# Optimization experiments

Measured on AMD Instinct MI355X. Metric: run time of the kernel, lower is better.

Reference implementation:

```python
import jax, jax.numpy as jnp
import numpy as np

B, L, D = 4096, 200, 128


def setup_inputs() -> dict:
    key = jax.random.key(0)
    ks = jax.random.split(key, 9)
    s_in = 1.0 / np.sqrt(2 * D)  # torch Linear default init scale (uniform bound)
    inp = {
        "h_states": jax.random.normal(ks[0], (B, L, D), dtype=jnp.float32),
        "target_emb_proj": jax.random.normal(ks[1], (B, D), dtype=jnp.float32),
        "mask": jax.random.randint(ks[2], (B, L), 0, 2).astype(bool),
        "W_r": jax.random.uniform(ks[3], (2 * D, D), jnp.float32, -s_in, s_in),
        "b_r": jax.random.uniform(ks[4], (D,), jnp.float32, -s_in, s_in),
        "W_u": jax.random.uniform(ks[5], (2 * D, D), jnp.float32, -s_in, s_in),
        "b_u": jax.random.uniform(ks[6], (D,), jnp.float32, -s_in, s_in),
        "W_h": jax.random.uniform(ks[7], (2 * D, D), jnp.float32, -s_in, s_in),
        "b_h": jax.random.uniform(ks[8], (D,), jnp.float32, -s_in, s_in),
    }
    return inp


def reference(h_states, target_emb_proj, mask, W_r, b_r, W_u, b_u, W_h, b_h):
    Bd, Ld, Dd = h_states.shape
    # target-aware attention scores over history: (B, L)
    scores = jnp.einsum("bld,bd->bl", h_states, target_emb_proj) / np.sqrt(Dd).astype(h_states.dtype)
    scores = jnp.where(mask, scores, jnp.asarray(-1e9, scores.dtype))
    attn = jax.nn.softmax(scores, axis=-1)  # (B, L)

    xs = (
        jnp.transpose(h_states, (1, 0, 2)),  # (L, B, D)
        attn.T,                               # (L, B)
        mask.T,                               # (L, B)
    )

    def step(h, x):
        x_t, e_t, m_t = x
        combined = jnp.concatenate([x_t, h], axis=-1)  # (B, 2D)
        r = jax.nn.sigmoid(combined @ W_r + b_r)
        u = jax.nn.sigmoid(combined @ W_u + b_u)
        u_prime = e_t[:, None] * u
        h_tilde = jnp.tanh(jnp.concatenate([x_t, r * h], axis=-1) @ W_h + b_h)
        h_new = (1.0 - u_prime) * h + u_prime * h_tilde
        h_next = jnp.where(m_t[:, None], h_new, h)
        return h_next, None

    h0 = jnp.zeros((Bd, Dd), dtype=h_states.dtype)
    h_final, _ = jax.lax.scan(step, h0, xs)
    return h_final
```

## Files before the change

### kernel.cpp

```cpp
#include <hip/hip_runtime.h>
#include <hip/hip_bf16.h>
#include <stdint.h>

#define LSEQ 200
#define DDIM 128

typedef __attribute__((ext_vector_type(8))) __bf16 bf16x8;
typedef __attribute__((ext_vector_type(4))) float f32x4;

__device__ __forceinline__ float fast_exp(float x) {
  return __builtin_amdgcn_exp2f(x * 1.4426950408889634f);
}
__device__ __forceinline__ float fast_sigmoid(float x) {
  return __builtin_amdgcn_rcpf(1.0f + fast_exp(-x));
}
__device__ __forceinline__ float fast_tanh(float x) {
  float ax = __builtin_fabsf(x);
  float t = __builtin_amdgcn_exp2f(ax * -2.885390081777927f);
  float r = (1.0f - t) * __builtin_amdgcn_rcpf(1.0f + t);
  return x < 0.0f ? -r : r;
}
__device__ __forceinline__ f32x4 mfma16(bf16x8 a, bf16x8 b, f32x4 c) {
  return __builtin_amdgcn_mfma_f32_16x16x32_bf16(a, b, c, 0, 0, 0);
}

__global__ __launch_bounds__(512) void k_scores(
    const float* __restrict__ h_states, const float* __restrict__ target,
    const int* __restrict__ mask, uint4* __restrict__ xp,
    float* __restrict__ attnT, int B) {
  __shared__ float s_sc[4][16][LSEQ];
  __shared__ float s_tgt[16][DDIM];
  const int b16 = blockIdx.x;
  const int bb = b16 * 16;
  const int tid = threadIdx.x;
  for (int i = tid; i < 16 * DDIM; i += 512)
    s_tgt[i >> 7][i & 127] = target[(size_t)(bb + (i >> 7)) * DDIM + (i & 127)];
  __syncthreads();

  {
    const int lane = tid & 63;
    const int kt = (tid >> 6) & 3;
    const int tp = tid >> 8;
    const int row = lane & 15;
    const int hi = lane >> 4;
    const int kbase = kt * 32 + hi * 8;
    const float* src = h_states + ((size_t)(bb + row) * LSEQ) * DDIM + kbase;
    const float* tg = &s_tgt[row][kbase];
#pragma unroll 2
    for (int t = tp; t < LSEQ; t += 2) {
      float4 a = *(const float4*)(src + (size_t)t * DDIM);
      float4 b = *(const float4*)(src + (size_t)t * DDIM + 4);
      float dv = (a.x * tg[0] + a.y * tg[1] + a.z * tg[2] + a.w * tg[3]) +
                 (b.x * tg[4] + b.y * tg[5] + b.z * tg[6] + b.w * tg[7]);
      dv += __shfl_xor(dv, 16);
      dv += __shfl_xor(dv, 32);
      if (hi == 0) s_sc[kt][row][t] = dv;
      union { __bf16 h[8]; uint4 v; } pk;
      pk.h[0] = (__bf16)a.x; pk.h[1] = (__bf16)a.y; pk.h[2] = (__bf16)a.z; pk.h[3] = (__bf16)a.w;
      pk.h[4] = (__bf16)b.x; pk.h[5] = (__bf16)b.y; pk.h[6] = (__bf16)b.z; pk.h[7] = (__bf16)b.w;
      xp[(((size_t)b16 * LSEQ + t) * 4 + kt) * 64 + lane] = pk.v;
    }
  }
  __syncthreads();

  if (tid < 256) {
    const int r2 = tid >> 4;
    const int j = tid & 15;
    const int* mrow = mask + (size_t)(bb + r2) * LSEQ;
    float mx = -3.0e38f;
    for (int t = j; t < LSEQ; t += 16) {
      float s = (s_sc[0][r2][t] + s_sc[1][r2][t]) + (s_sc[2][r2][t] + s_sc[3][r2][t]);
      s *= 0.088388347648318447f;
      s = (mrow[t] != 0) ? s : -3.0e38f;
      s_sc[0][r2][t] = s;
      mx = fmaxf(mx, s);
    }
    mx = fmaxf(mx, __shfl_xor(mx, 1));
    mx = fmaxf(mx, __shfl_xor(mx, 2));
    mx = fmaxf(mx, __shfl_xor(mx, 4));
    mx = fmaxf(mx, __shfl_xor(mx, 8));
    float se = 0.0f;
    for (int t = j; t < LSEQ; t += 16) {
      float e = fast_exp(s_sc[0][r2][t] - mx);
      s_sc[1][r2][t] = e;
      se += e;
    }
    se += __shfl_xor(se, 1);
    se += __shfl_xor(se, 2);
    se += __shfl_xor(se, 4);
    se += __shfl_xor(se, 8);
    float rs = __builtin_amdgcn_rcpf(se);
    for (int t = j; t < LSEQ; t += 16)
      attnT[((size_t)b16 * LSEQ + t) * 16 + r2] =
          (mrow[t] != 0) ? s_sc[1][r2][t] * rs : 0.0f;
  }
}

#define STEP(t, XC, XN, AXRC, AXUC, AXHC, AXRN, AXUN, AXHN)                  \
  do {                                                                       \
    if ((t) + 2 < LSEQ) {                                                    \
      _Pragma("unroll") for (int kt = 0; kt < 4; ++kt)                       \
          XN[kt] = xpb[((size_t)(t) + 2) * 256 + kt * 64];                   \
    }                                                                        \
    float att = s_att[(t)][rA];                                              \
    bf16x8 hf[4];                                                            \
    _Pragma("unroll") for (int kt = 0; kt < 4; ++kt)                         \
        hf[kt] = __builtin_bit_cast(bf16x8, s_hb_f[kt][lane]);               \
    if ((t) + 1 < LSEQ) {         \
      AXRN = vbr;                                                            \
      AXUN = vbu;                                                            \
      _Pragma("unroll") for (int kt = 0; kt < 4; ++kt) {                     \
        bf16x8 b = __builtin_bit_cast(bf16x8, XC[kt]);                       \
        AXRN = mfma16(wr[kt], b, AXRN);                                      \
        AXUN = mfma16(wu[kt], b, AXUN);                                      \
      }                                                                      \
    }                                                                        \
    f32x4 r1 = AXRC, u1 = AXUC;                                              \
    f32x4 r2 = {0.f, 0.f, 0.f, 0.f}, u2 = {0.f, 0.f, 0.f, 0.f};              \
    r1 = mfma16(wr[4], hf[0], r1); u1 = mfma16(wu[4], hf[0], u1);            \
    r2 = mfma16(wr[6], hf[2], r2); u2 = mfma16(wu[6], hf[2], u2);            \
    r1 = mfma16(wr[5], hf[1], r1); u1 = mfma16(wu[5], hf[1], u1);            \
    r2 = mfma16(wr[7], hf[3], r2); u2 = mfma16(wu[7], hf[3], u2);            \
    f32x4 accr = r1 + r2, accu = u1 + u2;                                    \
    float rr[4], uu[4];                                                      \
    union { __bf16 h[4]; uint2 v; } rhv;                                     \
    _Pragma("unroll") for (int j = 0; j < 4; ++j) {                          \
      rr[j] = fast_sigmoid(accr[j]);                                         \
      uu[j] = fast_sigmoid(accu[j]);                                         \
      rhv.h[j] = (__bf16)(rr[j] * hD[j]);                                    \
    }                                                                        \
    *rh_w = rhv.v;                                                           \
    asm volatile("s_waitcnt lgkmcnt(0)" ::: "memory");                       \
    __builtin_amdgcn_s_barrier();                                            \
    __builtin_amdgcn_sched_barrier(0);                                       \
    bf16x8 rf[4];                                                            \
    _Pragma("unroll") for (int kt = 0; kt < 4; ++kt)                         \
        rf[kt] = __builtin_bit_cast(bf16x8, s_rh_f[kt][lane]);               \
    if ((t) + 1 < LSEQ) {                                                    \
      AXHN = vbh;                                                            \
      _Pragma("unroll") for (int kt = 0; kt < 4; ++kt)                       \
          AXHN = mfma16(wh[kt], __builtin_bit_cast(bf16x8, XC[kt]), AXHN);   \
    }                                                                        \
    f32x4 h1 = AXHC, h2 = {0.f, 0.f, 0.f, 0.f};                              \
    h1 = mfma16(wh[4], rf[0], h1);                                           \
    h2 = mfma16(wh[6], rf[2], h2);                                           \
    h1 = mfma16(wh[5], rf[1], h1);                                           \
    h2 = mfma16(wh[7], rf[3], h2);                                           \
    f32x4 acch = h1 + h2;                                                    \
    union { __bf16 h[4]; uint2 v; } hbv;                                     \
    _Pragma("unroll") for (int j = 0; j < 4; ++j) {                          \
      float ht = fast_tanh(acch[j]);                                         \
      float up = att * uu[j];                                                \
      hD[j] += up * (ht - hD[j]);                                            \
      hbv.h[j] = (__bf16)hD[j];                                              \
    }                                                                        \
    *hb_w = hbv.v;                                                           \
    asm volatile("s_waitcnt lgkmcnt(0)" ::: "memory");                       \
    __builtin_amdgcn_s_barrier();                                            \
    __builtin_amdgcn_sched_barrier(0);                                       \
  } while (0)

__global__ __launch_bounds__(512, 2) void k_recur(
    const uint4* __restrict__ xp, const float* __restrict__ attnT,
    const float* __restrict__ Wr, const float* __restrict__ br,
    const float* __restrict__ Wu, const float* __restrict__ bu,
    const float* __restrict__ Wh, const float* __restrict__ bh,
    float* __restrict__ out, int B) {
  __shared__ uint4 s_hb_f[4][64];
  __shared__ uint4 s_rh_f[4][64];
  __shared__ float s_att[LSEQ][16];
  const int tid = threadIdx.x;
  const int lane = tid & 63;
  const int wv = tid >> 6;
  const int b16 = blockIdx.x;
  const int bb = b16 * 16;
  const int q = lane >> 4;
  const int rA = lane & 15;
  const int col = wv * 16 + rA;

  bf16x8 wr[8], wu[8], wh[8];
#pragma unroll
  for (int kt = 0; kt < 8; ++kt) {
    bf16x8 tr, tu, th;
    int krow = kt * 32 + q * 8;
#pragma unroll
    for (int j = 0; j < 8; ++j) {
      tr[j] = (__bf16)Wr[(size_t)(krow + j) * DDIM + col];
      tu[j] = (__bf16)Wu[(size_t)(krow + j) * DDIM + col];
      th[j] = (__bf16)Wh[(size_t)(krow + j) * DDIM + col];
    }
    wr[kt] = tr; wu[kt] = tu; wh[kt] = th;
  }
  const int cbase = wv * 16 + q * 4;
  f32x4 vbr = {br[cbase], br[cbase + 1], br[cbase + 2], br[cbase + 3]};
  f32x4 vbu = {bu[cbase], bu[cbase + 1], bu[cbase + 2], bu[cbase + 3]};
  f32x4 vbh = {bh[cbase], bh[cbase + 1], bh[cbase + 2], bh[cbase + 3]};

  for (int i = tid; i < LSEQ * 16; i += 512)
    s_att[i >> 4][i & 15] = attnT[(size_t)b16 * LSEQ * 16 + i];
  if (tid < 256) s_hb_f[0][tid & 255] = (uint4){0, 0, 0, 0};

  const int lane_w = rA + 16 * ((wv & 1) * 2 + (q >> 1));
  uint2* hb_w = (uint2*)((char*)s_hb_f + (wv >> 1) * 1024 + lane_w * 16 + (q & 1) * 8);
  uint2* rh_w = (uint2*)((char*)s_rh_f + (wv >> 1) * 1024 + lane_w * 16 + (q & 1) * 8);

  const uint4* xpb = xp + (size_t)b16 * LSEQ * 256 + lane;

  uint4 xT[4], xA[4], xB[4];
#pragma unroll
  for (int kt = 0; kt < 4; ++kt) xT[kt] = xpb[kt * 64];
#pragma unroll
  for (int kt = 0; kt < 4; ++kt) xA[kt] = xpb[256 + kt * 64];
  f32x4 axr0 = vbr, axu0 = vbu, axh0 = vbh;
#pragma unroll
  for (int kt = 0; kt < 4; ++kt) {
    bf16x8 b = __builtin_bit_cast(bf16x8, xT[kt]);
    axr0 = mfma16(wr[kt], b, axr0);
    axu0 = mfma16(wu[kt], b, axu0);
    axh0 = mfma16(wh[kt], b, axh0);
  }
  f32x4 axr1, axu1, axh1;
  float hD[4] = {0.f, 0.f, 0.f, 0.f};
  __syncthreads();

  for (int t = 0; t < LSEQ; t += 2) {
    STEP(t, xA, xB, axr0, axu0, axh0, axr1, axu1, axh1);
    STEP(t + 1, xB, xA, axr1, axu1, axh1, axr0, axu0, axh0);
  }

  float4 o = {hD[0], hD[1], hD[2], hD[3]};
  *(float4*)(out + (size_t)(bb + rA) * DDIM + cbase) = o;
}

extern "C" void kernel_launch(void* const* d_in, const int* in_sizes, int n_in,
                              void* d_out, int out_size, void* d_ws, size_t ws_size,
                              hipStream_t stream) {
  const float* h_states = (const float*)d_in[0];
  const float* target   = (const float*)d_in[1];
  const int*   mask     = (const int*)d_in[2];
  const float* Wr = (const float*)d_in[3];
  const float* br = (const float*)d_in[4];
  const float* Wu = (const float*)d_in[5];
  const float* bu = (const float*)d_in[6];
  const float* Wh = (const float*)d_in[7];
  const float* bh = (const float*)d_in[8];

  const int B = in_sizes[0] / (LSEQ * DDIM);
  uint4* xp = (uint4*)d_ws;
  float* attnT = (float*)((char*)d_ws + (size_t)B * LSEQ * DDIM * 2);

  k_scores<<<B / 16, 512, 0, stream>>>(h_states, target, mask, xp, attnT, B);
  k_recur<<<B / 16, 512, 0, stream>>>(xp, attnT, Wr, br, Wu, bu, Wh, bh,
                                      (float*)d_out, B);
}
```

Baseline: 341.5 us.

## Deepen x prefetch to four steps and interleave input MFMAs around barriers

Grows the register prefetch ring for the input sequence from two to four timesteps so global loads have more steps to land. The input-projection MFMAs for the next step are split so half run before the r*h LDS write and half before the barrier, and the u sigmoid moves after the barrier. Boundary conditionals are dropped in favour of clamped redundant loads and unconditional MFMAs. The scheduler barriers are replaced with a plain compiler memory fence, which lets the compiler move work across the sync point. The cost is higher register pressure at 2 waves per SIMD and some wasted work on the final steps.

```diff
diff --git a/kernel.cpp b/kernel.cpp
--- a/kernel.cpp
+++ b/kernel.cpp
@@ -96,25 +96,29 @@
   }
 }
 
+#define LGKM_BARRIER()                                 \
+  asm volatile("s_waitcnt lgkmcnt(0)" ::: "memory");   \
+  __builtin_amdgcn_s_barrier();                        \
+  asm volatile("" ::: "memory")
+
 #define STEP(t, XC, XN, AXRC, AXUC, AXHC, AXRN, AXUN, AXHN)                  \
   do {                                                                       \
-    if ((t) + 2 < LSEQ) {                                                    \
-      _Pragma("unroll") for (int kt = 0; kt < 4; ++kt)                       \
-          XN[kt] = xpb[((size_t)(t) + 2) * 256 + kt * 64];                   \
-    }                                                                        \
+                                                      \
+    const int tl = ((t) + 4 < LSEQ) ? (t) + 4 : LSEQ - 4;                    \
+    _Pragma("unroll") for (int kt = 0; kt < 4; ++kt)                         \
+        XN[kt] = xpb[(size_t)tl * 256 + kt * 64];                            \
     float att = s_att[(t)][rA];                                              \
     bf16x8 hf[4];                                                            \
     _Pragma("unroll") for (int kt = 0; kt < 4; ++kt)                         \
         hf[kt] = __builtin_bit_cast(bf16x8, s_hb_f[kt][lane]);               \
-    if ((t) + 1 < LSEQ) {         \
-      AXRN = vbr;                                                            \
-      AXUN = vbu;                                                            \
-      _Pragma("unroll") for (int kt = 0; kt < 4; ++kt) {                     \
-        bf16x8 b = __builtin_bit_cast(bf16x8, XC[kt]);                       \
-        AXRN = mfma16(wr[kt], b, AXRN);                                      \
-        AXUN = mfma16(wu[kt], b, AXUN);                                      \
-      }                                                                      \
+                      \
+    AXRN = vbr; AXUN = vbu;                                                  \
+    _Pragma("unroll") for (int kt = 0; kt < 2; ++kt) {                       \
+      bf16x8 b = __builtin_bit_cast(bf16x8, XC[kt]);                         \
+      AXRN = mfma16(wr[kt], b, AXRN);                                        \
+      AXUN = mfma16(wu[kt], b, AXUN);                                        \
     }                                                                        \
+                               \
     f32x4 r1 = AXRC, u1 = AXUC;                                              \
     f32x4 r2 = {0.f, 0.f, 0.f, 0.f}, u2 = {0.f, 0.f, 0.f, 0.f};              \
     r1 = mfma16(wr[4], hf[0], r1); u1 = mfma16(wu[4], hf[0], u1);            \
@@ -122,25 +126,29 @@
     r1 = mfma16(wr[5], hf[1], r1); u1 = mfma16(wu[5], hf[1], u1);            \
     r2 = mfma16(wr[7], hf[3], r2); u2 = mfma16(wu[7], hf[3], u2);            \
     f32x4 accr = r1 + r2, accu = u1 + u2;                                    \
-    float rr[4], uu[4];                                                      \
     union { __bf16 h[4]; uint2 v; } rhv;                                     \
-    _Pragma("unroll") for (int j = 0; j < 4; ++j) {                          \
-      rr[j] = fast_sigmoid(accr[j]);                                         \
+    _Pragma("unroll") for (int j = 0; j < 4; ++j)                            \
+      rhv.h[j] = (__bf16)(fast_sigmoid(accr[j]) * hD[j]);                    \
+    *rh_w = rhv.v;                                                           \
+               \
+    _Pragma("unroll") for (int kt = 2; kt < 4; ++kt) {                       \
+      bf16x8 b = __builtin_bit_cast(bf16x8, XC[kt]);                         \
+      AXRN = mfma16(wr[kt], b, AXRN);                                        \
+      AXUN = mfma16(wu[kt], b, AXUN);                                        \
+    }                                                                        \
+    LGKM_BARRIER();                                                          \
+                                                      \
+    bf16x8 rf[4];                                                            \
+    _Pragma("unroll") for (int kt = 0; kt < 4; ++kt)                         \
+        rf[kt] = __builtin_bit_cast(bf16x8, s_rh_f[kt][lane]);               \
+                        \
+    float uu[4];                                                             \
+    _Pragma("unroll") for (int j = 0; j < 4; ++j)                            \
       uu[j] = fast_sigmoid(accu[j]);                                         \
-      rhv.h[j] = (__bf16)(rr[j] * hD[j]);                                    \
-    }                                                                        \
-    *rh_w = rhv.v;                                                           \
-    asm volatile("s_waitcnt lgkmcnt(0)" ::: "memory");                       \
-    __builtin_amdgcn_s_barrier();                                            \
-    __builtin_amdgcn_sched_barrier(0);                                       \
-    bf16x8 rf[4];                                                            \
-    _Pragma("unroll") for (int kt = 0; kt < 4; ++kt)                         \
-        rf[kt] = __builtin_bit_cast(bf16x8, s_rh_f[kt][lane]);               \
-    if ((t) + 1 < LSEQ) {                                                    \
-      AXHN = vbh;                                                            \
-      _Pragma("unroll") for (int kt = 0; kt < 4; ++kt)                       \
-          AXHN = mfma16(wh[kt], __builtin_bit_cast(bf16x8, XC[kt]), AXHN);   \
-    }                                                                        \
+    AXHN = vbh;                                                              \
+    _Pragma("unroll") for (int kt = 0; kt < 4; ++kt)                         \
+        AXHN = mfma16(wh[kt], __builtin_bit_cast(bf16x8, XC[kt]), AXHN);     \
+                                              \
     f32x4 h1 = AXHC, h2 = {0.f, 0.f, 0.f, 0.f};                              \
     h1 = mfma16(wh[4], rf[0], h1);                                           \
     h2 = mfma16(wh[6], rf[2], h2);                                           \
@@ -155,9 +163,7 @@
       hbv.h[j] = (__bf16)hD[j];                                              \
     }                                                                        \
     *hb_w = hbv.v;                                                           \
-    asm volatile("s_waitcnt lgkmcnt(0)" ::: "memory");                       \
-    __builtin_amdgcn_s_barrier();                                            \
-    __builtin_amdgcn_sched_barrier(0);                                       \
+    LGKM_BARRIER();                                                          \
   } while (0)
 
 __global__ __launch_bounds__(512, 2) void k_recur(
@@ -206,15 +212,20 @@
 
   const uint4* xpb = xp + (size_t)b16 * LSEQ * 256 + lane;
 
-  uint4 xT[4], xA[4], xB[4];
-#pragma unroll
-  for (int kt = 0; kt < 4; ++kt) xT[kt] = xpb[kt * 64];
-#pragma unroll
-  for (int kt = 0; kt < 4; ++kt) xA[kt] = xpb[256 + kt * 64];
+  uint4 xb0[4], xb1[4], xb2[4], xb3[4];
+#pragma unroll
+  for (int kt = 0; kt < 4; ++kt) xb0[kt] = xpb[kt * 64];
+#pragma unroll
+  for (int kt = 0; kt < 4; ++kt) xb1[kt] = xpb[256 + kt * 64];
+#pragma unroll
+  for (int kt = 0; kt < 4; ++kt) xb2[kt] = xpb[512 + kt * 64];
+#pragma unroll
+  for (int kt = 0; kt < 4; ++kt) xb3[kt] = xpb[768 + kt * 64];
+
   f32x4 axr0 = vbr, axu0 = vbu, axh0 = vbh;
 #pragma unroll
   for (int kt = 0; kt < 4; ++kt) {
-    bf16x8 b = __builtin_bit_cast(bf16x8, xT[kt]);
+    bf16x8 b = __builtin_bit_cast(bf16x8, xb0[kt]);
     axr0 = mfma16(wr[kt], b, axr0);
     axu0 = mfma16(wu[kt], b, axu0);
     axh0 = mfma16(wh[kt], b, axh0);
@@ -223,9 +234,11 @@
   float hD[4] = {0.f, 0.f, 0.f, 0.f};
   __syncthreads();
 
-  for (int t = 0; t < LSEQ; t += 2) {
-    STEP(t, xA, xB, axr0, axu0, axh0, axr1, axu1, axh1);
-    STEP(t + 1, xB, xA, axr1, axu1, axh1, axr0, axu0, axh0);
+  for (int t = 0; t < LSEQ; t += 4) {
+    STEP(t + 0, xb1, xb0, axr0, axu0, axh0, axr1, axu1, axh1);
+    STEP(t + 1, xb2, xb1, axr1, axu1, axh1, axr0, axu0, axh0);
+    STEP(t + 2, xb3, xb2, axr0, axu0, axh0, axr1, axu1, axh1);
+    STEP(t + 3, xb0, xb3, axr1, axu1, axh1, axr0, axu0, axh0);
   }
 
   float4 o = {hD[0], hD[1], hD[2], hD[3]};
```

After: 318.2 us. -6.8%, faster.

## Process two independent 16-row batch groups per block to interleave recurrences

Applied to the files above, without the earlier changes.

Each recurrence block now handles 32 batch rows as two independent 16-row chains, issuing their MFMAs interleaved so one chain's work can hide the other's latency within each barrier-separated step. This halves the grid size and the number of barriers per batch row. The input-projection MFMAs are no longer precomputed one step ahead; instead the x loads are prefetched two steps ahead in place. The cost is higher register pressure, fewer blocks (128 instead of 256 on a large GPU), and possible occupancy loss under the 512x2 launch bounds.

```diff
diff --git a/kernel.cpp b/kernel.cpp
--- a/kernel.cpp
+++ b/kernel.cpp
@@ -96,68 +96,85 @@
   }
 }
 
-#define STEP(t, XC, XN, AXRC, AXUC, AXHC, AXRN, AXUN, AXHN)                  \
+#define LGKM_BARRIER()                                 \
+  asm volatile("s_waitcnt lgkmcnt(0)" ::: "memory");   \
+  __builtin_amdgcn_s_barrier();                        \
+  asm volatile("" ::: "memory")
+
+#define STEP(t, XC0, XC1)                                                    \
   do {                                                                       \
-    if ((t) + 2 < LSEQ) {                                                    \
-      _Pragma("unroll") for (int kt = 0; kt < 4; ++kt)                       \
-          XN[kt] = xpb[((size_t)(t) + 2) * 256 + kt * 64];                   \
-    }                                                                        \
-    float att = s_att[(t)][rA];                                              \
-    bf16x8 hf[4];                                                            \
-    _Pragma("unroll") for (int kt = 0; kt < 4; ++kt)                         \
-        hf[kt] = __builtin_bit_cast(bf16x8, s_hb_f[kt][lane]);               \
-    if ((t) + 1 < LSEQ) {         \
-      AXRN = vbr;                                                            \
-      AXUN = vbu;                                                            \
+    float att0 = s_att[(t)][rA];                                             \
+    float att1 = s_att[(t)][16 + rA];                                        \
+    bf16x8 hf0[4], hf1[4];                                                   \
+    _Pragma("unroll") for (int kt = 0; kt < 4; ++kt) {                       \
+      hf0[kt] = __builtin_bit_cast(bf16x8, s_hb_f[0][kt][lane]);             \
+      hf1[kt] = __builtin_bit_cast(bf16x8, s_hb_f[1][kt][lane]);             \
+    }                                                                        \
+    f32x4 r0a = vbr, u0a = vbu, r1a = vbr, u1a = vbu;                        \
+    _Pragma("unroll") for (int kt = 0; kt < 4; ++kt) {   \
+      bf16x8 b0 = __builtin_bit_cast(bf16x8, XC0[kt]);                       \
+      bf16x8 b1 = __builtin_bit_cast(bf16x8, XC1[kt]);                       \
+      r0a = mfma16(wr[kt], b0, r0a);                                         \
+      u0a = mfma16(wu[kt], b0, u0a);                                         \
+      r1a = mfma16(wr[kt], b1, r1a);                                         \
+      u1a = mfma16(wu[kt], b1, u1a);                                         \
+    }                                                                        \
+    f32x4 r0b = {0.f,0.f,0.f,0.f}, u0b = {0.f,0.f,0.f,0.f};                  \
+    f32x4 r1b = {0.f,0.f,0.f,0.f}, u1b = {0.f,0.f,0.f,0.f};                  \
+    _Pragma("unroll") for (int kt = 0; kt < 4; ++kt) {           \
+      r0b = mfma16(wr[4 + kt], hf0[kt], r0b);                                \
+      u0b = mfma16(wu[4 + kt], hf0[kt], u0b);                                \
+      r1b = mfma16(wr[4 + kt], hf1[kt], r1b);                                \
+      u1b = mfma16(wu[4 + kt], hf1[kt], u1b);                                \
+    }                                                                        \
+    f32x4 accr0 = r0a + r0b, accu0 = u0a + u0b;                              \
+    f32x4 accr1 = r1a + r1b, accu1 = u1a + u1b;                              \
+    float uu0[4], uu1[4];                                                    \
+    union { __bf16 h[4]; uint2 v; } rhv0, rhv1;                              \
+    _Pragma("unroll") for (int j = 0; j < 4; ++j) {                          \
+      rhv0.h[j] = (__bf16)(fast_sigmoid(accr0[j]) * hD0[j]);                 \
+      rhv1.h[j] = (__bf16)(fast_sigmoid(accr1[j]) * hD1[j]);                 \
+      uu0[j] = fast_sigmoid(accu0[j]);                                       \
+      uu1[j] = fast_sigmoid(accu1[j]);                                       \
+    }                                                                        \
+    *rh_w0 = rhv0.v;                                                         \
+    *rh_w1 = rhv1.v;                                                         \
+    LGKM_BARRIER();                                                          \
+    bf16x8 rf0[4], rf1[4];                                                   \
+    _Pragma("unroll") for (int kt = 0; kt < 4; ++kt) {                       \
+      rf0[kt] = __builtin_bit_cast(bf16x8, s_rh_f[0][kt][lane]);             \
+      rf1[kt] = __builtin_bit_cast(bf16x8, s_rh_f[1][kt][lane]);             \
+    }                                                                        \
+    f32x4 h0a = vbh, h1a = vbh;                                              \
+    _Pragma("unroll") for (int kt = 0; kt < 4; ++kt) {   \
+      h0a = mfma16(wh[kt], __builtin_bit_cast(bf16x8, XC0[kt]), h0a);        \
+      h1a = mfma16(wh[kt], __builtin_bit_cast(bf16x8, XC1[kt]), h1a);        \
+    }                                                                        \
+    {         \
+      const int tl = ((t) + 2 < LSEQ) ? (t) + 2 : LSEQ - 1;                  \
       _Pragma("unroll") for (int kt = 0; kt < 4; ++kt) {                     \
-        bf16x8 b = __builtin_bit_cast(bf16x8, XC[kt]);                       \
-        AXRN = mfma16(wr[kt], b, AXRN);                                      \
-        AXUN = mfma16(wu[kt], b, AXUN);                                      \
+        XC0[kt] = xpb0[(size_t)tl * 256 + kt * 64];                          \
+        XC1[kt] = xpb1[(size_t)tl * 256 + kt * 64];                          \
       }                                                                      \
     }                                                                        \
-    f32x4 r1 = AXRC, u1 = AXUC;                                              \
-    f32x4 r2 = {0.f, 0.f, 0.f, 0.f}, u2 = {0.f, 0.f, 0.f, 0.f};              \
-    r1 = mfma16(wr[4], hf[0], r1); u1 = mfma16(wu[4], hf[0], u1);            \
-    r2 = mfma16(wr[6], hf[2], r2); u2 = mfma16(wu[6], hf[2], u2);            \
-    r1 = mfma16(wr[5], hf[1], r1); u1 = mfma16(wu[5], hf[1], u1);            \
-    r2 = mfma16(wr[7], hf[3], r2); u2 = mfma16(wu[7], hf[3], u2);            \
-    f32x4 accr = r1 + r2, accu = u1 + u2;                                    \
-    float rr[4], uu[4];                                                      \
-    union { __bf16 h[4]; uint2 v; } rhv;                                     \
+    f32x4 h0b = {0.f,0.f,0.f,0.f}, h1b = {0.f,0.f,0.f,0.f};                  \
+    _Pragma("unroll") for (int kt = 0; kt < 4; ++kt) {           \
+      h0b = mfma16(wh[4 + kt], rf0[kt], h0b);                                \
+      h1b = mfma16(wh[4 + kt], rf1[kt], h1b);                                \
+    }                                                                        \
+    f32x4 acch0 = h0a + h0b, acch1 = h1a + h1b;                              \
+    union { __bf16 h[4]; uint2 v; } hbv0, hbv1;                              \
     _Pragma("unroll") for (int j = 0; j < 4; ++j) {                          \
-      rr[j] = fast_sigmoid(accr[j]);                                         \
-      uu[j] = fast_sigmoid(accu[j]);                                         \
-      rhv.h[j] = (__bf16)(rr[j] * hD[j]);                                    \
-    }                                                                        \
-    *rh_w = rhv.v;                                                           \
-    asm volatile("s_waitcnt lgkmcnt(0)" ::: "memory");                       \
-    __builtin_amdgcn_s_barrier();                                            \
-    __builtin_amdgcn_sched_barrier(0);                                       \
-    bf16x8 rf[4];                                                            \
-    _Pragma("unroll") for (int kt = 0; kt < 4; ++kt)                         \
-        rf[kt] = __builtin_bit_cast(bf16x8, s_rh_f[kt][lane]);               \
-    if ((t) + 1 < LSEQ) {                                                    \
-      AXHN = vbh;                                                            \
-      _Pragma("unroll") for (int kt = 0; kt < 4; ++kt)                       \
-          AXHN = mfma16(wh[kt], __builtin_bit_cast(bf16x8, XC[kt]), AXHN);   \
-    }                                                                        \
-    f32x4 h1 = AXHC, h2 = {0.f, 0.f, 0.f, 0.f};                              \
-    h1 = mfma16(wh[4], rf[0], h1);                                           \
-    h2 = mfma16(wh[6], rf[2], h2);                                           \
-    h1 = mfma16(wh[5], rf[1], h1);                                           \
-    h2 = mfma16(wh[7], rf[3], h2);                                           \
-    f32x4 acch = h1 + h2;                                                    \
-    union { __bf16 h[4]; uint2 v; } hbv;                                     \
-    _Pragma("unroll") for (int j = 0; j < 4; ++j) {                          \
-      float ht = fast_tanh(acch[j]);                                         \
-      float up = att * uu[j];                                                \
-      hD[j] += up * (ht - hD[j]);                                            \
-      hbv.h[j] = (__bf16)hD[j];                                              \
-    }                                                                        \
-    *hb_w = hbv.v;                                                           \
-    asm volatile("s_waitcnt lgkmcnt(0)" ::: "memory");                       \
-    __builtin_amdgcn_s_barrier();                                            \
-    __builtin_amdgcn_sched_barrier(0);                                       \
+      float up0 = att0 * uu0[j];                                             \
+      hD0[j] += up0 * (fast_tanh(acch0[j]) - hD0[j]);                        \
+      hbv0.h[j] = (__bf16)hD0[j];                                            \
+      float up1 = att1 * uu1[j];                                             \
+      hD1[j] += up1 * (fast_tanh(acch1[j]) - hD1[j]);                        \
+      hbv1.h[j] = (__bf16)hD1[j];                                            \
+    }                                                                        \
+    *hb_w0 = hbv0.v;                                                         \
+    *hb_w1 = hbv1.v;                                                         \
+    LGKM_BARRIER();                                                          \
   } while (0)
 
 __global__ __launch_bounds__(512, 2) void k_recur(
@@ -166,14 +183,14 @@
     const float* __restrict__ Wu, const float* __restrict__ bu,
     const float* __restrict__ Wh, const float* __restrict__ bh,
     float* __restrict__ out, int B) {
-  __shared__ uint4 s_hb_f[4][64];
-  __shared__ uint4 s_rh_f[4][64];
-  __shared__ float s_att[LSEQ][16];
+  __shared__ uint4 s_hb_f[2][4][64];
+  __shared__ uint4 s_rh_f[2][4][64];
+  __shared__ float s_att[LSEQ][32];
   const int tid = threadIdx.x;
   const int lane = tid & 63;
   const int wv = tid >> 6;
-  const int b16 = blockIdx.x;
-  const int bb = b16 * 16;
+  const int b32 = blockIdx.x;
+  const int bb = b32 * 32;
   const int q = lane >> 4;
   const int rA = lane & 15;
   const int col = wv * 16 + rA;
@@ -196,40 +213,43 @@
   f32x4 vbu = {bu[cbase], bu[cbase + 1], bu[cbase + 2], bu[cbase + 3]};
   f32x4 vbh = {bh[cbase], bh[cbase + 1], bh[cbase + 2], bh[cbase + 3]};
 
-  for (int i = tid; i < LSEQ * 16; i += 512)
-    s_att[i >> 4][i & 15] = attnT[(size_t)b16 * LSEQ * 16 + i];
-  if (tid < 256) s_hb_f[0][tid & 255] = (uint4){0, 0, 0, 0};
-
-  const int lane_w = rA + 16 * ((wv & 1) * 2 + (q >> 1));
-  uint2* hb_w = (uint2*)((char*)s_hb_f + (wv >> 1) * 1024 + lane_w * 16 + (q & 1) * 8);
-  uint2* rh_w = (uint2*)((char*)s_rh_f + (wv >> 1) * 1024 + lane_w * 16 + (q & 1) * 8);
-
-  const uint4* xpb = xp + (size_t)b16 * LSEQ * 256 + lane;
-
-  uint4 xT[4], xA[4], xB[4];
-#pragma unroll
-  for (int kt = 0; kt < 4; ++kt) xT[kt] = xpb[kt * 64];
-#pragma unroll
-  for (int kt = 0; kt < 4; ++kt) xA[kt] = xpb[256 + kt * 64];
-  f32x4 axr0 = vbr, axu0 = vbu, axh0 = vbh;
+  for (int i = tid; i < LSEQ * 32; i += 512) {
+    int t = i >> 5, gr = (i >> 4) & 1, r = i & 15;
+    s_att[t][gr * 16 + r] =
+        attnT[((size_t)(b32 * 2 + gr) * LSEQ + t) * 16 + r];
+  }
+  ((uint4*)s_hb_f)[tid] = (uint4){0, 0, 0, 0};
+
+  const int w_off = (wv >> 1) * 1024 + (rA + 16 * ((wv & 1) * 2 + (q >> 1))) * 16 + (q & 1) * 8;
+  uint2* hb_w0 = (uint2*)((char*)&s_hb_f[0][0][0] + w_off);
+  uint2* hb_w1 = (uint2*)((char*)&s_hb_f[1][0][0] + w_off);
+  uint2* rh_w0 = (uint2*)((char*)&s_rh_f[0][0][0] + w_off);
+  uint2* rh_w1 = (uint2*)((char*)&s_rh_f[1][0][0] + w_off);
+
+  const uint4* xpb0 = xp + (size_t)(b32 * 2) * LSEQ * 256 + lane;
+  const uint4* xpb1 = xp + (size_t)(b32 * 2 + 1) * LSEQ * 256 + lane;
+
+  uint4 xA0[4], xB0[4], xA1[4], xB1[4];
 #pragma unroll
   for (int kt = 0; kt < 4; ++kt) {
-    bf16x8 b = __builtin_bit_cast(bf16x8, xT[kt]);
-    axr0 = mfma16(wr[kt], b, axr0);
-    axu0 = mfma16(wu[kt], b, axu0);
-    axh0 = mfma16(wh[kt], b, axh0);
-  }
-  f32x4 axr1, axu1, axh1;
-  float hD[4] = {0.f, 0.f, 0.f, 0.f};
+    xA0[kt] = xpb0[kt * 64];
+    xA1[kt] = xpb1[kt * 64];
+    xB0[kt] = xpb0[256 + kt * 64];
+    xB1[kt] = xpb1[256 + kt * 64];
+  }
+  float hD0[4] = {0.f, 0.f, 0.f, 0.f};
+  float hD1[4] = {0.f, 0.f, 0.f, 0.f};
   __syncthreads();
 
   for (int t = 0; t < LSEQ; t += 2) {
-    STEP(t, xA, xB, axr0, axu0, axh0, axr1, axu1, axh1);
-    STEP(t + 1, xB, xA, axr1, axu1, axh1, axr0, axu0, axh0);
-  }
-
-  float4 o = {hD[0], hD[1], hD[2], hD[3]};
-  *(float4*)(out + (size_t)(bb + rA) * DDIM + cbase) = o;
+    STEP(t, xA0, xA1);
+    STEP(t + 1, xB0, xB1);
+  }
+
+  float4 o0 = {hD0[0], hD0[1], hD0[2], hD0[3]};
+  *(float4*)(out + (size_t)(bb + rA) * DDIM + cbase) = o0;
+  float4 o1 = {hD1[0], hD1[1], hD1[2], hD1[3]};
+  *(float4*)(out + (size_t)(bb + 16 + rA) * DDIM + cbase) = o1;
 }
 
 extern "C" void kernel_launch(void* const* d_in, const int* in_sizes, int n_in,
@@ -250,6 +270,6 @@
   float* attnT = (float*)((char*)d_ws + (size_t)B * LSEQ * DDIM * 2);
 
   k_scores<<<B / 16, 512, 0, stream>>>(h_states, target, mask, xp, attnT, B);
-  k_recur<<<B / 16, 512, 0, stream>>>(xp, attnT, Wr, br, Wu, bu, Wh, bh,
+  k_recur<<<B / 32, 512, 0, stream>>>(xp, attnT, Wr, br, Wu, bu, Wh, bh,
                                       (float*)d_out, B);
 }
```

Result: slower. 514.2 us (+50.6%).
